# Kernel tuning notes

Hardware: AMD Instinct MI355X
Metric: run time of the kernel (lower is better)

## Reference

```python
import jax, jax.numpy as jnp
import numpy as np

D_MODEL = 1024
NUM_HEADS = 16
D_K = D_MODEL // NUM_HEADS


def setup_inputs() -> dict:
    key = jax.random.key(0)
    ks = jax.random.split(key, 11)
    B, S = 4, 2048
    s = 1.0 / np.sqrt(D_MODEL)
    return {
        "q": jax.random.normal(ks[0], (B, S, D_MODEL), jnp.float32),
        "k": jax.random.normal(ks[1], (B, S, D_MODEL), jnp.float32),
        "v": jax.random.normal(ks[2], (B, S, D_MODEL), jnp.float32),
        "w_q": jax.random.normal(ks[3], (D_MODEL, D_MODEL), jnp.float32) * s,
        "b_q": jnp.zeros((D_MODEL,), jnp.float32),
        "w_k": jax.random.normal(ks[4], (D_MODEL, D_MODEL), jnp.float32) * s,
        "b_k": jnp.zeros((D_MODEL,), jnp.float32),
        "w_v": jax.random.normal(ks[5], (D_MODEL, D_MODEL), jnp.float32) * s,
        "b_v": jnp.zeros((D_MODEL,), jnp.float32),
        "w_o": jax.random.normal(ks[6], (D_MODEL, D_MODEL), jnp.float32) * s,
        "b_o": jnp.zeros((D_MODEL,), jnp.float32),
    }


def reference(q, k, v, w_q, b_q, w_k, b_k, w_v, b_v, w_o, b_o):
    B, S, _ = q.shape
    # projections; torch Linear computes x @ W.T + b
    def proj(x, w, b):
        y = x @ w.T + b
        return y.reshape(B, -1, NUM_HEADS, D_K).transpose(0, 2, 1, 3)  # (B,H,S,d_k)

    qh, kh, vh = proj(q, w_q, b_q), proj(k, w_k, b_k), proj(v, w_v, b_v)
    scores = jnp.einsum("bhqd,bhkd->bhqk", qh, kh) / jnp.sqrt(jnp.float32(D_K))
    attn_weights = jax.nn.softmax(scores, axis=-1)
    x = jnp.einsum("bhqk,bhkd->bhqd", attn_weights, vh)
    x = x.transpose(0, 2, 1, 3).reshape(B, -1, D_MODEL)
    out = x @ w_o.T + b_o
    return out, attn_weights
```

## Files before the change

### kernel.cpp

```cpp
#include <hip/hip_runtime.h>
#include <math.h>

#define S_LEN 2048
#define DM 1024
#define NH 16
#define DK 64

typedef __attribute__((ext_vector_type(8))) short short8;
typedef __attribute__((ext_vector_type(4))) short short4v;
typedef __attribute__((ext_vector_type(4))) float f32x4;

#define LGKM_BARRIER() do { \
    asm volatile("s_waitcnt lgkmcnt(0)" ::: "memory"); \
    __builtin_amdgcn_s_barrier(); \
    __builtin_amdgcn_sched_barrier(0); \
  } while (0)

__device__ __forceinline__ short f2bf(float f) {
  unsigned u = __builtin_bit_cast(unsigned, f);
  u = (u + 0x7FFFu + ((u >> 16) & 1u)) >> 16;
  return (short)u;
}

__device__ __forceinline__ void gld_lds16(const short* g, short* l) {
  __builtin_amdgcn_global_load_lds(
      (const __attribute__((address_space(1))) unsigned int*)g,
      (__attribute__((address_space(3))) unsigned int*)l, 16, 0, 0);
}

__global__ __launch_bounds__(256) void cvt_bf16(
    const float* __restrict__ s0, const float* __restrict__ s1,
    const float* __restrict__ s2, const float* __restrict__ s3,
    short* __restrict__ d0, short* __restrict__ d1,
    short* __restrict__ d2, short* __restrict__ d3, int n)
{
  const float* s; short* d;
  switch (blockIdx.y) {
    case 0:  s = s0; d = d0; break;
    case 1:  s = s1; d = d1; break;
    case 2:  s = s2; d = d2; break;
    default: s = s3; d = d3; break;
  }
  const int i = (blockIdx.x * 256 + threadIdx.x) * 8;
  if (i < n) {
    const float4 v0 = *(const float4*)&s[i];
    const float4 v1 = *(const float4*)&s[i + 4];
    short8 r = { f2bf(v0.x), f2bf(v0.y), f2bf(v0.z), f2bf(v0.w),
                 f2bf(v1.x), f2bf(v1.y), f2bf(v1.z), f2bf(v1.w) };
    *(short8*)&d[i] = r;
  }
}

__global__ __launch_bounds__(256) void proj3(
    const short* __restrict__ qb, const short* __restrict__ kb, const short* __restrict__ vb,
    const short* __restrict__ wqb, const short* __restrict__ wkb, const short* __restrict__ wvb,
    const float* __restrict__ biq, const float* __restrict__ bik, const float* __restrict__ biv,
    short* __restrict__ qhb, short* __restrict__ khb, short* __restrict__ vtb)
{
  __shared__ short SM[17408];
  short* As = SM;
  short* Bs = SM + 4096;

  const int z = blockIdx.z;
  const short* A; const short* B; const float* bias; short* o;
  if (z == 0)      { A = qb; B = wqb; bias = biq; o = qhb; }
  else if (z == 1) { A = kb; B = wkb; bias = bik; o = khb; }
  else             { A = vb; B = wvb; bias = biv; o = vtb; }

  const int tid = threadIdx.x;
  const int lane = tid & 63;
  const int wv = tid >> 6;
  const int grp = lane >> 4, lid = lane & 15;
  const int wr = wv >> 1, wc = wv & 1;
  const int bm = blockIdx.x, bn = blockIdx.y;

  f32x4 acc[4][4] = {};

  const int idx0 = tid, idx1 = 256 + tid;
  const int r0 = idx0 >> 2, c0 = (idx0 & 3) * 8;
  const int r1 = idx1 >> 2, c1 = (idx1 & 3) * 8;
  const short* a0 = &A[(size_t)(bm * 128 + r0) * DM + c0];
  const short* a1 = &A[(size_t)(bm * 128 + r1) * DM + c1];
  const short* b0 = &B[(size_t)(bn * 128 + r0) * DM + c0];
  const short* b1 = &B[(size_t)(bn * 128 + r1) * DM + c1];

  for (int ks = 0; ks < 32; ++ks) {
    __syncthreads();
    gld_lds16(a0 + ks * 32, &As[idx0 * 8]);
    gld_lds16(a1 + ks * 32, &As[idx1 * 8]);
    gld_lds16(b0 + ks * 32, &Bs[idx0 * 8]);
    gld_lds16(b1 + ks * 32, &Bs[idx1 * 8]);
    __syncthreads();
    short8 a[4], b[4];
    #pragma unroll
    for (int m = 0; m < 4; ++m) a[m] = *(const short8*)&As[(wr * 64 + m * 16 + lid) * 32 + grp * 8];
    #pragma unroll
    for (int n = 0; n < 4; ++n) b[n] = *(const short8*)&Bs[(wc * 64 + n * 16 + lid) * 32 + grp * 8];
    #pragma unroll
    for (int m = 0; m < 4; ++m)
      #pragma unroll
      for (int n = 0; n < 4; ++n)
        acc[m][n] = __builtin_amdgcn_mfma_f32_16x16x32_bf16(a[m], b[n], acc[m][n], 0, 0, 0);
  }

  if (z < 2) {
    #pragma unroll
    for (int n = 0; n < 4; ++n) {
      const int ng = bn * 128 + wc * 64 + n * 16 + lid;
      const float bvs = bias[ng];
      const int h = ng >> 6, d = ng & 63;
      #pragma unroll
      for (int m = 0; m < 4; ++m) {
        const int mg = bm * 128 + wr * 64 + m * 16 + grp * 4;
        const int bb = mg >> 11, s = mg & 2047;
        #pragma unroll
        for (int r = 0; r < 4; ++r)
          o[(((size_t)bb * NH + h) * S_LEN + s + r) * DK + d] = f2bf(acc[m][n][r] + bvs);
      }
    }
  } else {
    __syncthreads();
    #pragma unroll
    for (int n = 0; n < 4; ++n) {
      const int ngl = wc * 64 + n * 16 + lid;
      const float bvs = bias[bn * 128 + ngl];
      #pragma unroll
      for (int m = 0; m < 4; ++m) {
        const int sl = wr * 64 + m * 16 + grp * 4;
        short4v c4 = { f2bf(acc[m][n][0] + bvs), f2bf(acc[m][n][1] + bvs),
                       f2bf(acc[m][n][2] + bvs), f2bf(acc[m][n][3] + bvs) };
        *(short4v*)&SM[ngl * 136 + sl] = c4;
      }
    }
    __syncthreads();
    const int bb = bm >> 4, s0 = (bm & 15) * 128;
    #pragma unroll
    for (int i = 0; i < 8; ++i) {
      const int id = tid + 256 * i;
      const int row = id >> 4;
      const int c8 = (id & 15) * 8;
      const short8 vv = *(const short8*)&SM[row * 136 + c8];
      *(short8*)&o[((size_t)bb * 1024 + bn * 128 + row) * S_LEN + s0 + c8] = vv;
    }
  }
}

__global__ __launch_bounds__(256) void gemm_o(
    const short* __restrict__ A, const short* __restrict__ B,
    const float* __restrict__ bias, float* __restrict__ of)
{
  __shared__ short As[128 * 32];
  __shared__ short Bs[128 * 32];
  const int tid = threadIdx.x;
  const int lane = tid & 63;
  const int wv = tid >> 6;
  const int grp = lane >> 4, lid = lane & 15;
  const int wr = wv >> 1, wc = wv & 1;
  const int bm = blockIdx.x, bn = blockIdx.y;

  f32x4 acc[4][4] = {};

  const int idx0 = tid, idx1 = 256 + tid;
  const int r0 = idx0 >> 2, c0 = (idx0 & 3) * 8;
  const int r1 = idx1 >> 2, c1 = (idx1 & 3) * 8;
  const short* a0 = &A[(size_t)(bm * 128 + r0) * DM + c0];
  const short* a1 = &A[(size_t)(bm * 128 + r1) * DM + c1];
  const short* b0 = &B[(size_t)(bn * 128 + r0) * DM + c0];
  const short* b1 = &B[(size_t)(bn * 128 + r1) * DM + c1];

  for (int ks = 0; ks < 32; ++ks) {
    __syncthreads();
    gld_lds16(a0 + ks * 32, &As[idx0 * 8]);
    gld_lds16(a1 + ks * 32, &As[idx1 * 8]);
    gld_lds16(b0 + ks * 32, &Bs[idx0 * 8]);
    gld_lds16(b1 + ks * 32, &Bs[idx1 * 8]);
    __syncthreads();
    short8 a[4], b[4];
    #pragma unroll
    for (int m = 0; m < 4; ++m) a[m] = *(const short8*)&As[(wr * 64 + m * 16 + lid) * 32 + grp * 8];
    #pragma unroll
    for (int n = 0; n < 4; ++n) b[n] = *(const short8*)&Bs[(wc * 64 + n * 16 + lid) * 32 + grp * 8];
    #pragma unroll
    for (int m = 0; m < 4; ++m)
      #pragma unroll
      for (int n = 0; n < 4; ++n)
        acc[m][n] = __builtin_amdgcn_mfma_f32_16x16x32_bf16(a[m], b[n], acc[m][n], 0, 0, 0);
  }

  #pragma unroll
  for (int n = 0; n < 4; ++n) {
    const int ng = bn * 128 + wc * 64 + n * 16 + lid;
    const float bvs = bias[ng];
    #pragma unroll
    for (int m = 0; m < 4; ++m) {
      const int mg = bm * 128 + wr * 64 + m * 16 + grp * 4;
      #pragma unroll
      for (int r = 0; r < 4; ++r)
        __builtin_nontemporal_store(acc[m][n][r] + bvs, &of[(size_t)(mg + r) * DM + ng]);
    }
  }
}

__global__ __launch_bounds__(128) void mha_attn8(
    const short* __restrict__ qh, const short* __restrict__ kh, const short* __restrict__ vt,
    float* __restrict__ attn, short* __restrict__ xb)
{
  __shared__ short Kt[64][72];
  __shared__ short Vt[64][72];
  __shared__ short Ps[2][32][72];

  const int tid = threadIdx.x;
  const int lane = tid & 63, wv = tid >> 6, grp = lane >> 4, lid = lane & 15;

  const int nid = blockIdx.x;
  const int x = nid & 7, jj = nid >> 3;
  const int bh = x + 8 * (jj >> 5);
  const int qt = jj & 31;

  const size_t baseQ = (size_t)bh * S_LEN * DK;
  const size_t baseV = (size_t)bh * DK * S_LEN;
  const float scale2 = 0.18033688f;

  const short* Qb = qh + baseQ;
  const short* Kb = kh + baseQ;
  const short* Vb = vt + baseV;

  int tr[4], tc[4];
  #pragma unroll
  for (int i = 0; i < 4; ++i) {
    const int id = tid + 128 * i;
    tr[i] = id >> 3; tc[i] = (id & 7) * 8;
  }

  short8 aq[2][2];
  #pragma unroll
  for (int qb2 = 0; qb2 < 2; ++qb2)
    #pragma unroll
    for (int kf = 0; kf < 2; ++kf)
      aq[qb2][kf] = *(const short8*)&Qb[(size_t)(qt * 64 + wv * 32 + qb2 * 16 + lid) * DK + kf * 32 + grp * 8];

  float lsum[2] = {};

  short8 kr[4];
  #pragma unroll
  for (int i = 0; i < 4; ++i) kr[i] = *(const short8*)&Kb[(size_t)tr[i] * DK + tc[i]];
  for (int kt = 0; kt < 32; ++kt) {
    short* buf = (kt & 1) ? &Ps[0][0][0] : &Kt[0][0];
    #pragma unroll
    for (int i = 0; i < 4; ++i) *(short8*)&buf[tr[i] * 72 + tc[i]] = kr[i];
    if (kt < 31) {
      #pragma unroll
      for (int i = 0; i < 4; ++i)
        kr[i] = *(const short8*)&Kb[(size_t)((kt + 1) * 64 + tr[i]) * DK + tc[i]];
    }
    LGKM_BARRIER();
    f32x4 sacc[4][2] = {};
    __builtin_amdgcn_s_setprio(1);
    #pragma unroll
    for (int kf = 0; kf < 2; ++kf) {
      short8 ak[4];
      #pragma unroll
      for (int kb2 = 0; kb2 < 4; ++kb2) ak[kb2] = *(const short8*)&buf[(kb2 * 16 + lid) * 72 + kf * 32 + grp * 8];
      #pragma unroll
      for (int kb2 = 0; kb2 < 4; ++kb2)
        #pragma unroll
        for (int qb2 = 0; qb2 < 2; ++qb2)
          sacc[kb2][qb2] = __builtin_amdgcn_mfma_f32_16x16x32_bf16(ak[kb2], aq[qb2][kf], sacc[kb2][qb2], 0, 0, 0);
    }
    __builtin_amdgcn_s_setprio(0);
    #pragma unroll
    for (int qb2 = 0; qb2 < 2; ++qb2)
      #pragma unroll
      for (int kb2 = 0; kb2 < 4; ++kb2)
        #pragma unroll
        for (int r = 0; r < 4; ++r)
          lsum[qb2] += __builtin_amdgcn_exp2f(sacc[kb2][qb2][r] * scale2);
  }

  float log2l[2];
  #pragma unroll
  for (int qb2 = 0; qb2 < 2; ++qb2) {
    float s = lsum[qb2];
    s += __shfl_xor(s, 16);
    s += __shfl_xor(s, 32);
    log2l[qb2] = __log2f(s);
  }

  f32x4 oacc[2][4] = {};
  float* attnB = attn + ((size_t)bh * S_LEN + qt * 64 + wv * 32) * S_LEN;

  short8 vr[4];
  #pragma unroll
  for (int i = 0; i < 4; ++i) {
    kr[i] = *(const short8*)&Kb[(size_t)tr[i] * DK + tc[i]];
    vr[i] = *(const short8*)&Vb[(size_t)tr[i] * S_LEN + tc[i]];
  }
  for (int kt = 0; kt < 32; ++kt) {
    LGKM_BARRIER();
    #pragma unroll
    for (int i = 0; i < 4; ++i) {
      *(short8*)&Kt[tr[i]][tc[i]] = kr[i];
      *(short8*)&Vt[tr[i]][tc[i]] = vr[i];
    }
    if (kt < 31) {
      #pragma unroll
      for (int i = 0; i < 4; ++i) {
        kr[i] = *(const short8*)&Kb[(size_t)((kt + 1) * 64 + tr[i]) * DK + tc[i]];
        vr[i] = *(const short8*)&Vb[(size_t)tr[i] * S_LEN + (kt + 1) * 64 + tc[i]];
      }
    }
    LGKM_BARRIER();

    f32x4 sacc[4][2] = {};
    __builtin_amdgcn_s_setprio(1);
    #pragma unroll
    for (int kf = 0; kf < 2; ++kf) {
      short8 ak[4];
      #pragma unroll
      for (int kb2 = 0; kb2 < 4; ++kb2) ak[kb2] = *(const short8*)&Kt[kb2 * 16 + lid][kf * 32 + grp * 8];
      #pragma unroll
      for (int kb2 = 0; kb2 < 4; ++kb2)
        #pragma unroll
        for (int qb2 = 0; qb2 < 2; ++qb2)
          sacc[kb2][qb2] = __builtin_amdgcn_mfma_f32_16x16x32_bf16(ak[kb2], aq[qb2][kf], sacc[kb2][qb2], 0, 0, 0);
    }
    __builtin_amdgcn_s_setprio(0);

    #pragma unroll
    for (int qb2 = 0; qb2 < 2; ++qb2) {
      const float nl = -log2l[qb2];
      #pragma unroll
      for (int kb2 = 0; kb2 < 4; ++kb2) {
        short4v p4;
        #pragma unroll
        for (int r = 0; r < 4; ++r)
          p4[r] = f2bf(__builtin_amdgcn_exp2f(__builtin_fmaf(sacc[kb2][qb2][r], scale2, nl)));
        *(short4v*)&Ps[wv][qb2 * 16 + lid][kb2 * 16 + grp * 4] = p4;
      }
    }

    __builtin_amdgcn_s_setprio(1);
    #pragma unroll
    for (int kf = 0; kf < 2; ++kf) {
      short8 ap[2], bvv[4];
      #pragma unroll
      for (int mf = 0; mf < 2; ++mf) ap[mf] = *(const short8*)&Ps[wv][mf * 16 + lid][kf * 32 + grp * 8];
      #pragma unroll
      for (int nf = 0; nf < 4; ++nf) bvv[nf] = *(const short8*)&Vt[nf * 16 + lid][kf * 32 + grp * 8];
      #pragma unroll
      for (int mf = 0; mf < 2; ++mf)
        #pragma unroll
        for (int nf = 0; nf < 4; ++nf)
          oacc[mf][nf] = __builtin_amdgcn_mfma_f32_16x16x32_bf16(ap[mf], bvv[nf], oacc[mf][nf], 0, 0, 0);
    }
    __builtin_amdgcn_s_setprio(0);

    #pragma unroll
    for (int i = 0; i < 8; ++i) {
      const int qrow = i * 4 + grp;
      const uint2 u = *(const uint2*)&Ps[wv][qrow][lid * 4];
      f32x4 f;
      f[0] = __builtin_bit_cast(float, u.x << 16);
      f[1] = __builtin_bit_cast(float, u.x & 0xffff0000u);
      f[2] = __builtin_bit_cast(float, u.y << 16);
      f[3] = __builtin_bit_cast(float, u.y & 0xffff0000u);
      __builtin_nontemporal_store(f, (f32x4*)&attnB[(size_t)qrow * S_LEN + kt * 64 + lid * 4]);
    }
  }

  const int b = bh >> 4, h = bh & 15;
  #pragma unroll
  for (int mf = 0; mf < 2; ++mf) {
    #pragma unroll
    for (int nf = 0; nf < 4; ++nf) {
      #pragma unroll
      for (int r = 0; r < 4; ++r) {
        const int s = qt * 64 + wv * 32 + mf * 16 + grp * 4 + r;
        const int d = nf * 16 + lid;
        xb[((size_t)b * S_LEN + s) * DM + h * DK + d] = f2bf(oacc[mf][nf][r]);
      }
    }
  }
}

template<int MODE>
__global__ __launch_bounds__(256) void mha_gemm(
    const float* __restrict__ Af, const short* __restrict__ Ab,
    const float* __restrict__ W, const float* __restrict__ bias,
    short* __restrict__ obf, float* __restrict__ of)
{
  __shared__ short As[128][40];
  __shared__ short Bs[128][40];
  const int tid = threadIdx.x;
  const int lane = tid & 63, wv = tid >> 6;
  const int grp = lane >> 4, lid = lane & 15;
  const int wr = wv >> 1, wc = wv & 1;
  const int bm = blockIdx.x, bn = blockIdx.y;

  f32x4 acc[4][4] = {};

  for (int ks = 0; ks < 32; ++ks) {
    __syncthreads();
    if (MODE == 0) {
      #pragma unroll
      for (int i = 0; i < 4; ++i) {
        const int c = tid + 256 * i;
        const int row = c >> 3, kc = c & 7;
        const float4 v = *(const float4*)&Af[(size_t)(bm * 128 + row) * DM + ks * 32 + kc * 4];
        short4v s4 = { f2bf(v.x), f2bf(v.y), f2bf(v.z), f2bf(v.w) };
        *(short4v*)&As[row][kc * 4] = s4;
      }
    } else {
      #pragma unroll
      for (int i = 0; i < 2; ++i) {
        const int c = tid + 256 * i;
        const int row = c >> 2, k8 = (c & 3) * 8;
        *(float4*)&As[row][k8] = *(const float4*)&Ab[(size_t)(bm * 128 + row) * DM + ks * 32 + k8];
      }
    }
    #pragma unroll
    for (int i = 0; i < 4; ++i) {
      const int c = tid + 256 * i;
      const int row = c >> 3, kc = c & 7;
      const float4 v = *(const float4*)&W[(size_t)(bn * 128 + row) * DM + ks * 32 + kc * 4];
      short4v s4 = { f2bf(v.x), f2bf(v.y), f2bf(v.z), f2bf(v.w) };
      *(short4v*)&Bs[row][kc * 4] = s4;
    }
    __syncthreads();
    short8 a[4], b[4];
    #pragma unroll
    for (int m = 0; m < 4; ++m) a[m] = *(const short8*)&As[wr * 64 + m * 16 + lid][grp * 8];
    #pragma unroll
    for (int n = 0; n < 4; ++n) b[n] = *(const short8*)&Bs[wc * 64 + n * 16 + lid][grp * 8];
    #pragma unroll
    for (int m = 0; m < 4; ++m)
      #pragma unroll
      for (int n = 0; n < 4; ++n)
        acc[m][n] = __builtin_amdgcn_mfma_f32_16x16x32_bf16(a[m], b[n], acc[m][n], 0, 0, 0);
  }

  #pragma unroll
  for (int n = 0; n < 4; ++n) {
    const int ng = bn * 128 + wc * 64 + n * 16 + lid;
    const float bvs = bias[ng];
    #pragma unroll
    for (int m = 0; m < 4; ++m) {
      const int mg = bm * 128 + wr * 64 + m * 16 + grp * 4;
      #pragma unroll
      for (int r = 0; r < 4; ++r) {
        const float val = acc[m][n][r] + bvs;
        const int mm = mg + r;
        if (MODE == 0) {
          const int bb = mm >> 11, s = mm & 2047, h = ng >> 6, d = ng & 63;
          obf[(((size_t)bb * NH + h) * S_LEN + s) * DK + d] = f2bf(val);
        } else {
          of[(size_t)mm * DM + ng] = val;
        }
      }
    }
  }
}

__global__ __launch_bounds__(256) void mha_attn_old(
    const short* __restrict__ qh, const short* __restrict__ kh, const short* __restrict__ vh,
    float* __restrict__ attn, short* __restrict__ xb)
{
  __shared__ short QP[128][72];
  __shared__ short Ks[64][72];
  __shared__ short VT[64][72];

  const int tid = threadIdx.x;
  const int lane = tid & 63, wv = tid >> 6, grp = lane >> 4, lid = lane & 15;
  const int qt = blockIdx.x, bh = blockIdx.y;
  const size_t base = (size_t)bh * S_LEN * DK;
  const float scale = 0.125f;

  #pragma unroll
  for (int i = 0; i < 4; ++i) {
    const int c = tid + 256 * i;
    const int row = c >> 3, k8 = (c & 7) * 8;
    *(float4*)&QP[row][k8] = *(const float4*)&qh[base + (size_t)(qt * 128 + row) * DK + k8];
  }
  __syncthreads();
  short8 aq[2][2];
  #pragma unroll
  for (int mf = 0; mf < 2; ++mf)
    #pragma unroll
    for (int kf = 0; kf < 2; ++kf)
      aq[mf][kf] = *(const short8*)&QP[wv * 32 + mf * 16 + lid][kf * 32 + grp * 8];

  float lsum[2][4] = {};

  for (int kt = 0; kt < 32; ++kt) {
    __syncthreads();
    #pragma unroll
    for (int i = 0; i < 2; ++i) {
      const int c = tid + 256 * i;
      const int row = c >> 3, k8 = (c & 7) * 8;
      *(float4*)&Ks[row][k8] = *(const float4*)&kh[base + (size_t)(kt * 64 + row) * DK + k8];
    }
    __syncthreads();
    f32x4 sacc[2][4] = {};
    #pragma unroll
    for (int kf = 0; kf < 2; ++kf) {
      short8 bk[4];
      #pragma unroll
      for (int nf = 0; nf < 4; ++nf) bk[nf] = *(const short8*)&Ks[nf * 16 + lid][kf * 32 + grp * 8];
      #pragma unroll
      for (int mf = 0; mf < 2; ++mf)
        #pragma unroll
        for (int nf = 0; nf < 4; ++nf)
          sacc[mf][nf] = __builtin_amdgcn_mfma_f32_16x16x32_bf16(aq[mf][kf], bk[nf], sacc[mf][nf], 0, 0, 0);
    }
    #pragma unroll
    for (int mf = 0; mf < 2; ++mf)
      #pragma unroll
      for (int r = 0; r < 4; ++r)
        #pragma unroll
        for (int nf = 0; nf < 4; ++nf)
          lsum[mf][r] += __expf(sacc[mf][nf][r] * scale);
  }

  float rl[2][4];
  #pragma unroll
  for (int mf = 0; mf < 2; ++mf)
    #pragma unroll
    for (int r = 0; r < 4; ++r) {
      float s = lsum[mf][r];
      #pragma unroll
      for (int off = 8; off >= 1; off >>= 1) s += __shfl_xor(s, off, 16);
      rl[mf][r] = 1.f / s;
    }

  f32x4 oacc[2][4] = {};

  for (int kt = 0; kt < 32; ++kt) {
    __syncthreads();
    #pragma unroll
    for (int i = 0; i < 2; ++i) {
      const int c = tid + 256 * i;
      const int row = c >> 3, k8 = (c & 7) * 8;
      *(float4*)&Ks[row][k8] = *(const float4*)&kh[base + (size_t)(kt * 64 + row) * DK + k8];
    }
    #pragma unroll
    for (int i = 0; i < 2; ++i) {
      const int key = tid & 63;
      const int d0 = ((tid >> 6) << 3) + i * 32;
      const float4 v = *(const float4*)&vh[base + (size_t)(kt * 64 + key) * DK + d0];
      const short8 sv = __builtin_bit_cast(short8, v);
      #pragma unroll
      for (int jj = 0; jj < 8; ++jj) VT[d0 + jj][key] = sv[jj];
    }
    __syncthreads();
    f32x4 sacc[2][4] = {};
    #pragma unroll
    for (int kf = 0; kf < 2; ++kf) {
      short8 bk[4];
      #pragma unroll
      for (int nf = 0; nf < 4; ++nf) bk[nf] = *(const short8*)&Ks[nf * 16 + lid][kf * 32 + grp * 8];
      #pragma unroll
      for (int mf = 0; mf < 2; ++mf)
        #pragma unroll
        for (int nf = 0; nf < 4; ++nf)
          sacc[mf][nf] = __builtin_amdgcn_mfma_f32_16x16x32_bf16(aq[mf][kf], bk[nf], sacc[mf][nf], 0, 0, 0);
    }
    #pragma unroll
    for (int mf = 0; mf < 2; ++mf) {
      #pragma unroll
      for (int nf = 0; nf < 4; ++nf) {
        #pragma unroll
        for (int r = 0; r < 4; ++r) {
          const float p = __expf(sacc[mf][nf][r] * scale) * rl[mf][r];
          const int qr = wv * 32 + mf * 16 + grp * 4 + r;
          const int kc = kt * 64 + nf * 16 + lid;
          attn[((size_t)bh * S_LEN + qt * 128 + qr) * S_LEN + kc] = p;
          QP[wv * 32 + (qr & 31)][nf * 16 + lid] = f2bf(p);
        }
      }
    }
    #pragma unroll
    for (int kf = 0; kf < 2; ++kf) {
      short8 ap[2], bvv[4];
      #pragma unroll
      for (int mf = 0; mf < 2; ++mf) ap[mf] = *(const short8*)&QP[wv * 32 + mf * 16 + lid][kf * 32 + grp * 8];
      #pragma unroll
      for (int nf = 0; nf < 4; ++nf) bvv[nf] = *(const short8*)&VT[nf * 16 + lid][kf * 32 + grp * 8];
      #pragma unroll
      for (int mf = 0; mf < 2; ++mf)
        #pragma unroll
        for (int nf = 0; nf < 4; ++nf)
          oacc[mf][nf] = __builtin_amdgcn_mfma_f32_16x16x32_bf16(ap[mf], bvv[nf], oacc[mf][nf], 0, 0, 0);
    }
  }

  const int b = bh >> 4, h = bh & 15;
  #pragma unroll
  for (int mf = 0; mf < 2; ++mf) {
    #pragma unroll
    for (int nf = 0; nf < 4; ++nf) {
      #pragma unroll
      for (int r = 0; r < 4; ++r) {
        const int s = qt * 128 + wv * 32 + mf * 16 + grp * 4 + r;
        const int d = nf * 16 + lid;
        xb[((size_t)b * S_LEN + s) * DM + h * DK + d] = f2bf(oacc[mf][nf][r]);
      }
    }
  }
}

extern "C" void kernel_launch(void* const* d_in, const int* in_sizes, int n_in,
                              void* d_out, int out_size, void* d_ws, size_t ws_size,
                              hipStream_t stream) {
  const float* q  = (const float*)d_in[0];
  const float* k  = (const float*)d_in[1];
  const float* v  = (const float*)d_in[2];
  const float* wq = (const float*)d_in[3];
  const float* bq = (const float*)d_in[4];
  const float* wk = (const float*)d_in[5];
  const float* bk = (const float*)d_in[6];
  const float* wv = (const float*)d_in[7];
  const float* bv = (const float*)d_in[8];
  const float* wo = (const float*)d_in[9];
  const float* bo = (const float*)d_in[10];

  float* out  = (float*)d_out;
  float* attn = out + (size_t)4 * S_LEN * DM;

  const size_t NTOK = (size_t)4 * S_LEN * DM;
  const size_t NW   = (size_t)DM * DM;
  dim3 blk(256);

  if (ws_size >= 135000000ull) {
    short* qb  = (short*)d_ws;
    short* kb  = qb + NTOK;
    short* vb  = kb + NTOK;
    short* wqb = vb + NTOK;
    short* wkb = wqb + NW;
    short* wvb = wkb + NW;
    short* wob = wvb + NW;
    short* qhb = wob + NW;
    short* khb = qhb + NTOK;
    short* vtb = khb + NTOK;
    short* xb  = vtb + NTOK;

    cvt_bf16<<<dim3(4096, 3), blk, 0, stream>>>(q, k, v, (const float*)nullptr,
                                                qb, kb, vb, (short*)nullptr, (int)NTOK);
    cvt_bf16<<<dim3(512, 4), blk, 0, stream>>>(wq, wk, wv, wo, wqb, wkb, wvb, wob, (int)NW);

    proj3<<<dim3(64, 8, 3), blk, 0, stream>>>(qb, kb, vb, wqb, wkb, wvb, bq, bk, bv,
                                              qhb, khb, vtb);

    mha_attn8<<<dim3(2048), dim3(128), 0, stream>>>(qhb, khb, vtb, attn, xb);

    gemm_o<<<dim3(64, 8), blk, 0, stream>>>(xb, wob, bo, out);
  } else {
    short* qhb = (short*)d_ws;
    short* khb = qhb + NTOK;
    short* vhb = khb + NTOK;
    short* xb  = vhb + NTOK;

    mha_gemm<0><<<dim3(64, 8), blk, 0, stream>>>(q, (const short*)nullptr, wq, bq, qhb, (float*)nullptr);
    mha_gemm<0><<<dim3(64, 8), blk, 0, stream>>>(k, (const short*)nullptr, wk, bk, khb, (float*)nullptr);
    mha_gemm<0><<<dim3(64, 8), blk, 0, stream>>>(v, (const short*)nullptr, wv, bv, vhb, (float*)nullptr);
    mha_attn_old<<<dim3(16, 64), blk, 0, stream>>>(qhb, khb, vhb, attn, xb);
    mha_gemm<1><<<dim3(64, 8), blk, 0, stream>>>((const float*)nullptr, xb, wo, bo, (short*)nullptr, out);
  }
}
```

Measured before the change: 385.6 us.

## Give each wave private K/V/P LDS tiles and drop block barriers in attention

```diff
diff --git a/kernel.cpp b/kernel.cpp
--- a/kernel.cpp
+++ b/kernel.cpp
@@ -9,12 +9,6 @@
 typedef __attribute__((ext_vector_type(8))) short short8;
 typedef __attribute__((ext_vector_type(4))) short short4v;
 typedef __attribute__((ext_vector_type(4))) float f32x4;
-
-#define LGKM_BARRIER() do { \
-    asm volatile("s_waitcnt lgkmcnt(0)" ::: "memory"); \
-    __builtin_amdgcn_s_barrier(); \
-    __builtin_amdgcn_sched_barrier(0); \
-  } while (0)
 
 __device__ __forceinline__ short f2bf(float f) {
   unsigned u = __builtin_bit_cast(unsigned, f);
@@ -201,13 +195,13 @@
   }
 }
 
-__global__ __launch_bounds__(128) void mha_attn8(
+__global__ __launch_bounds__(128) void mha_attn9(
     const short* __restrict__ qh, const short* __restrict__ kh, const short* __restrict__ vt,
     float* __restrict__ attn, short* __restrict__ xb)
 {
-  __shared__ short Kt[64][72];
-  __shared__ short Vt[64][72];
-  __shared__ short Ps[2][32][72];
+  __shared__ short Kt[2][32][72];
+  __shared__ short Vt[2][64][40];
+  __shared__ short Ps[2][32][40];
 
   const int tid = threadIdx.x;
   const int lane = tid & 63, wv = tid >> 6, grp = lane >> 4, lid = lane & 15;
@@ -225,11 +219,12 @@
   const short* Kb = kh + baseQ;
   const short* Vb = vt + baseV;
 
-  int tr[4], tc[4];
+  int trk[4], tck[4], trv[4], tcv[4];
   #pragma unroll
   for (int i = 0; i < 4; ++i) {
-    const int id = tid + 128 * i;
-    tr[i] = id >> 3; tc[i] = (id & 7) * 8;
+    const int c = lane + 64 * i;
+    trk[i] = c >> 3;  tck[i] = (c & 7) * 8;
+    trv[i] = c >> 2;  tcv[i] = (c & 3) * 8;
   }
 
   short8 aq[2][2];
@@ -243,26 +238,24 @@
 
   short8 kr[4];
   #pragma unroll
-  for (int i = 0; i < 4; ++i) kr[i] = *(const short8*)&Kb[(size_t)tr[i] * DK + tc[i]];
-  for (int kt = 0; kt < 32; ++kt) {
-    short* buf = (kt & 1) ? &Ps[0][0][0] : &Kt[0][0];
-    #pragma unroll
-    for (int i = 0; i < 4; ++i) *(short8*)&buf[tr[i] * 72 + tc[i]] = kr[i];
-    if (kt < 31) {
+  for (int i = 0; i < 4; ++i) kr[i] = *(const short8*)&Kb[(size_t)trk[i] * DK + tck[i]];
+  for (int kt = 0; kt < 64; ++kt) {
+    #pragma unroll
+    for (int i = 0; i < 4; ++i) *(short8*)&Kt[wv][trk[i]][tck[i]] = kr[i];
+    if (kt < 63) {
       #pragma unroll
       for (int i = 0; i < 4; ++i)
-        kr[i] = *(const short8*)&Kb[(size_t)((kt + 1) * 64 + tr[i]) * DK + tc[i]];
-    }
-    LGKM_BARRIER();
-    f32x4 sacc[4][2] = {};
+        kr[i] = *(const short8*)&Kb[(size_t)((kt + 1) * 32 + trk[i]) * DK + tck[i]];
+    }
+    f32x4 sacc[2][2] = {};
     __builtin_amdgcn_s_setprio(1);
     #pragma unroll
     for (int kf = 0; kf < 2; ++kf) {
-      short8 ak[4];
-      #pragma unroll
-      for (int kb2 = 0; kb2 < 4; ++kb2) ak[kb2] = *(const short8*)&buf[(kb2 * 16 + lid) * 72 + kf * 32 + grp * 8];
-      #pragma unroll
-      for (int kb2 = 0; kb2 < 4; ++kb2)
+      short8 ak[2];
+      #pragma unroll
+      for (int kb2 = 0; kb2 < 2; ++kb2) ak[kb2] = *(const short8*)&Kt[wv][kb2 * 16 + lid][kf * 32 + grp * 8];
+      #pragma unroll
+      for (int kb2 = 0; kb2 < 2; ++kb2)
         #pragma unroll
         for (int qb2 = 0; qb2 < 2; ++qb2)
           sacc[kb2][qb2] = __builtin_amdgcn_mfma_f32_16x16x32_bf16(ak[kb2], aq[qb2][kf], sacc[kb2][qb2], 0, 0, 0);
@@ -271,7 +264,7 @@
     #pragma unroll
     for (int qb2 = 0; qb2 < 2; ++qb2)
       #pragma unroll
-      for (int kb2 = 0; kb2 < 4; ++kb2)
+      for (int kb2 = 0; kb2 < 2; ++kb2)
         #pragma unroll
         for (int r = 0; r < 4; ++r)
           lsum[qb2] += __builtin_amdgcn_exp2f(sacc[kb2][qb2][r] * scale2);
@@ -292,34 +285,32 @@
   short8 vr[4];
   #pragma unroll
   for (int i = 0; i < 4; ++i) {
-    kr[i] = *(const short8*)&Kb[(size_t)tr[i] * DK + tc[i]];
-    vr[i] = *(const short8*)&Vb[(size_t)tr[i] * S_LEN + tc[i]];
-  }
-  for (int kt = 0; kt < 32; ++kt) {
-    LGKM_BARRIER();
+    kr[i] = *(const short8*)&Kb[(size_t)trk[i] * DK + tck[i]];
+    vr[i] = *(const short8*)&Vb[(size_t)trv[i] * S_LEN + tcv[i]];
+  }
+  for (int kt = 0; kt < 64; ++kt) {
     #pragma unroll
     for (int i = 0; i < 4; ++i) {
-      *(short8*)&Kt[tr[i]][tc[i]] = kr[i];
-      *(short8*)&Vt[tr[i]][tc[i]] = vr[i];
-    }
-    if (kt < 31) {
+      *(short8*)&Kt[wv][trk[i]][tck[i]] = kr[i];
+      *(short8*)&Vt[wv][trv[i]][tcv[i]] = vr[i];
+    }
+    if (kt < 63) {
       #pragma unroll
       for (int i = 0; i < 4; ++i) {
-        kr[i] = *(const short8*)&Kb[(size_t)((kt + 1) * 64 + tr[i]) * DK + tc[i]];
-        vr[i] = *(const short8*)&Vb[(size_t)tr[i] * S_LEN + (kt + 1) * 64 + tc[i]];
-      }
-    }
-    LGKM_BARRIER();
-
-    f32x4 sacc[4][2] = {};
+        kr[i] = *(const short8*)&Kb[(size_t)((kt + 1) * 32 + trk[i]) * DK + tck[i]];
+        vr[i] = *(const short8*)&Vb[(size_t)trv[i] * S_LEN + (kt + 1) * 32 + tcv[i]];
+      }
+    }
+
+    f32x4 sacc[2][2] = {};
     __builtin_amdgcn_s_setprio(1);
     #pragma unroll
     for (int kf = 0; kf < 2; ++kf) {
-      short8 ak[4];
-      #pragma unroll
-      for (int kb2 = 0; kb2 < 4; ++kb2) ak[kb2] = *(const short8*)&Kt[kb2 * 16 + lid][kf * 32 + grp * 8];
-      #pragma unroll
-      for (int kb2 = 0; kb2 < 4; ++kb2)
+      short8 ak[2];
+      #pragma unroll
+      for (int kb2 = 0; kb2 < 2; ++kb2) ak[kb2] = *(const short8*)&Kt[wv][kb2 * 16 + lid][kf * 32 + grp * 8];
+      #pragma unroll
+      for (int kb2 = 0; kb2 < 2; ++kb2)
         #pragma unroll
         for (int qb2 = 0; qb2 < 2; ++qb2)
           sacc[kb2][qb2] = __builtin_amdgcn_mfma_f32_16x16x32_bf16(ak[kb2], aq[qb2][kf], sacc[kb2][qb2], 0, 0, 0);
@@ -330,7 +321,7 @@
     for (int qb2 = 0; qb2 < 2; ++qb2) {
       const float nl = -log2l[qb2];
       #pragma unroll
-      for (int kb2 = 0; kb2 < 4; ++kb2) {
+      for (int kb2 = 0; kb2 < 2; ++kb2) {
         short4v p4;
         #pragma unroll
         for (int r = 0; r < 4; ++r)
@@ -340,13 +331,12 @@
     }
 
     __builtin_amdgcn_s_setprio(1);
-    #pragma unroll
-    for (int kf = 0; kf < 2; ++kf) {
+    {
       short8 ap[2], bvv[4];
       #pragma unroll
-      for (int mf = 0; mf < 2; ++mf) ap[mf] = *(const short8*)&Ps[wv][mf * 16 + lid][kf * 32 + grp * 8];
-      #pragma unroll
-      for (int nf = 0; nf < 4; ++nf) bvv[nf] = *(const short8*)&Vt[nf * 16 + lid][kf * 32 + grp * 8];
+      for (int mf = 0; mf < 2; ++mf) ap[mf] = *(const short8*)&Ps[wv][mf * 16 + lid][grp * 8];
+      #pragma unroll
+      for (int nf = 0; nf < 4; ++nf) bvv[nf] = *(const short8*)&Vt[wv][nf * 16 + lid][grp * 8];
       #pragma unroll
       for (int mf = 0; mf < 2; ++mf)
         #pragma unroll
@@ -356,15 +346,17 @@
     __builtin_amdgcn_s_setprio(0);
 
     #pragma unroll
-    for (int i = 0; i < 8; ++i) {
-      const int qrow = i * 4 + grp;
-      const uint2 u = *(const uint2*)&Ps[wv][qrow][lid * 4];
+    for (int i = 0; i < 4; ++i) {
+      const int c = lane + 64 * i;
+      const int qrow = c >> 3;
+      const int kc4 = (c & 7) * 4;
+      const uint2 u = *(const uint2*)&Ps[wv][qrow][kc4];
       f32x4 f;
       f[0] = __builtin_bit_cast(float, u.x << 16);
       f[1] = __builtin_bit_cast(float, u.x & 0xffff0000u);
       f[2] = __builtin_bit_cast(float, u.y << 16);
       f[3] = __builtin_bit_cast(float, u.y & 0xffff0000u);
-      __builtin_nontemporal_store(f, (f32x4*)&attnB[(size_t)qrow * S_LEN + kt * 64 + lid * 4]);
+      __builtin_nontemporal_store(f, (f32x4*)&attnB[(size_t)qrow * S_LEN + kt * 32 + kc4]);
     }
   }
 
@@ -650,7 +642,7 @@
     proj3<<<dim3(64, 8, 3), blk, 0, stream>>>(qb, kb, vb, wqb, wkb, wvb, bq, bk, bv,
                                               qhb, khb, vtb);
 
-    mha_attn8<<<dim3(2048), dim3(128), 0, stream>>>(qhb, khb, vtb, attn, xb);
+    mha_attn9<<<dim3(2048), dim3(128), 0, stream>>>(qhb, khb, vtb, attn, xb);
 
     gemm_o<<<dim3(64, 8), blk, 0, stream>>>(xb, wob, bo, out);
   } else {
```

Result: slower. 410.6 us (+6.5%).
